# Performance work log

Measured on AMD Instinct MI355X. Metric: run time of the kernel, lower is better.

Reference implementation:

```python
import jax, jax.numpy as jnp
import numpy as np

DIM = 2048
N_HEADS = 16
N_KV_HEADS = 4
HEAD_DIM = DIM // N_HEADS


def setup_inputs() -> dict:
    key = jax.random.key(0)
    k1, k2, k3, k4, k5 = jax.random.split(key, 5)
    B, T = 2, 2048
    scale = 1.0 / np.sqrt(DIM)
    x = jax.random.normal(k1, (B, T, DIM), dtype=jnp.float32)
    # weights stored as [in, out] so forward is x @ W (same math as nn.Linear)
    Wq = jax.random.normal(k2, (DIM, DIM), dtype=jnp.float32) * scale
    Wk = jax.random.normal(k3, (DIM, N_KV_HEADS * HEAD_DIM), dtype=jnp.float32) * scale
    Wv = jax.random.normal(k4, (DIM, N_KV_HEADS * HEAD_DIM), dtype=jnp.float32) * scale
    Wo = jax.random.normal(k5, (DIM, DIM), dtype=jnp.float32) * scale
    return {"x": x, "Wq": Wq, "Wk": Wk, "Wv": Wv, "Wo": Wo}


def reference(x, Wq, Wk, Wv, Wo):
    B, T, C = x.shape
    G = N_HEADS // N_KV_HEADS  # query heads per kv head
    # projections
    q = (x @ Wq).reshape(B, T, N_KV_HEADS, G, HEAD_DIM)   # [B,T,K,G,d]
    k = (x @ Wk).reshape(B, T, N_KV_HEADS, HEAD_DIM)      # [B,T,K,d]
    v = (x @ Wv).reshape(B, T, N_KV_HEADS, HEAD_DIM)      # [B,T,K,d]
    # attention scores: grouped heads share kv head (no repeat_interleave copy)
    att = jnp.einsum('btkgd,bskd->bkgts', q, k) / np.sqrt(HEAD_DIM)  # [B,K,G,T,T]
    att = jax.nn.softmax(att, axis=-1)
    out = jnp.einsum('bkgts,bskd->btkgd', att, v).reshape(B, T, C)
    return out @ Wo
```

## Files before the change

### kernel.cpp

```cpp
#include <hip/hip_runtime.h>
#include <hip/hip_bf16.h>

typedef __hip_bfloat16 bf16;
typedef __attribute__((ext_vector_type(8))) short short8;
typedef __attribute__((ext_vector_type(4))) short short4v;
typedef __attribute__((ext_vector_type(4))) float f32x4;

#define DIMC 2048
#define TSEQ 2048
#define NB 2
#define KVH 4
#define NH 16
#define HD 128
#define KVD 512
#define QSCALE 0.12751744f

__device__ __forceinline__ void mfma16(f32x4& acc, short8 a, short8 b) {
  acc = __builtin_amdgcn_mfma_f32_16x16x32_bf16(a, b, acc, 0, 0, 0);
}

__device__ __forceinline__ void gload_lds16(const bf16* g, bf16* l) {
  __builtin_amdgcn_global_load_lds(
      (const __attribute__((address_space(1))) void*)g,
      (__attribute__((address_space(3))) void*)l, 16, 0, 0);
}

__device__ __forceinline__ int swz(int row, int col) {
  return col ^ ((row & 7) << 3);
}

__global__ __launch_bounds__(256) void f2b(const float* __restrict__ in,
                                           bf16* __restrict__ out, long n4) {
  long i = (long)blockIdx.x * 256 + threadIdx.x;
  if (i >= n4) return;
  const f32x4 v = *(const f32x4*)(in + i * 4);
  union { short4v s; bf16 h[4]; } u;
#pragma unroll
  for (int j = 0; j < 4; ++j) u.h[j] = __float2bfloat16(v[j]);
  *(short4v*)(out + i * 4) = u.s;
}

__global__ __launch_bounds__(256) void transpose_w_f2b(const float* __restrict__ in,
                                                       bf16* __restrict__ out, int C,
                                                       float scale) {
  __shared__ bf16 tile[64][72];
  int rb = blockIdx.y * 64, cb = blockIdx.x * 64;
  int tx = threadIdx.x & 63, ty = threadIdx.x >> 6;
  for (int i = ty; i < 64; i += 4)
    tile[i][tx] = __float2bfloat16(in[(long)(rb + i) * C + cb + tx] * scale);
  __syncthreads();
  for (int i = ty; i < 64; i += 4)
    out[(long)(cb + i) * DIMC + rb + tx] = tile[tx][i];
}

#define GEMM_BODY(A_, Bt_, K_)                                                  \
  const int tid = threadIdx.x;                                                  \
  const int lane = tid & 63, wid = tid >> 6;                                    \
  const long m0 = blockIdx.y * 128, n0 = blockIdx.x * 128;                      \
  const int wm = (wid >> 1) * 64, wn = (wid & 1) * 64;                          \
  f32x4 acc[4][4] = {};                                                         \
  const int srow = lane >> 2, scol = (lane & 3) * 8;                            \
  const bf16* Ag = A_ + (m0 + srow) * (long)K_ + scol;                          \
  const bf16* Bg = Bt_ + (n0 + srow) * (long)K_ + scol;                         \
  for (int k0 = 0; k0 < K_; k0 += 32) {                                         \
    for (int p = 0; p < 2; ++p) {                                               \
      int rr = p * 64 + wid * 16;                                               \
      gload_lds16(Ag + (long)rr * K_ + k0, As + rr * 32);                       \
      gload_lds16(Bg + (long)rr * K_ + k0, Bs + rr * 32);                       \
    }                                                                           \
    __syncthreads();                                                            \
    const int ko = (lane >> 4) * 8;                                             \
    short8 af[4], bq[4];                                                        \
    _Pragma("unroll") for (int i = 0; i < 4; ++i) {                             \
      af[i] = *(const short8*)(As + (wm + i * 16 + (lane & 15)) * 32 + ko);     \
      bq[i] = *(const short8*)(Bs + (wn + i * 16 + (lane & 15)) * 32 + ko);     \
    }                                                                           \
    _Pragma("unroll") for (int i = 0; i < 4; ++i)                               \
      _Pragma("unroll") for (int j = 0; j < 4; ++j)                             \
        mfma16(acc[i][j], af[i], bq[j]);                                        \
    __syncthreads();                                                            \
  }                                                                             \
  const int cr = (lane >> 4) * 4, cc = lane & 15;

__global__ __launch_bounds__(256) void gemm_qkv(const bf16* __restrict__ A,
                                                const bf16* __restrict__ Bt,
                                                bf16* __restrict__ qp,
                                                bf16* __restrict__ kp,
                                                bf16* __restrict__ vT) {
  __shared__ bf16 As[128 * 32];
  __shared__ bf16 Bs[128 * 32];
  GEMM_BODY(A, Bt, 2048)
#pragma unroll
  for (int i = 0; i < 4; ++i)
#pragma unroll
    for (int j = 0; j < 4; ++j)
#pragma unroll
      for (int r = 0; r < 4; ++r) {
        long m = m0 + wm + i * 16 + cr + r;
        long n = n0 + wn + j * 16 + cc;
        float val = acc[i][j][r];
        if (n0 < 2048) {
          qp[m * DIMC + n] = __float2bfloat16(val);
        } else if (n0 < 2560) {
          kp[m * KVD + (n - 2048)] = __float2bfloat16(val);
        } else {
          long nn = n - 2560;
          long z = (m >> 11) * 4 + (nn >> 7);
          vT[z * (HD * (long)TSEQ) + (nn & 127) * (long)TSEQ + (m & 2047)] =
              __float2bfloat16(val);
        }
      }
}

__global__ __launch_bounds__(256) void gemm_out(const bf16* __restrict__ A,
                                                const bf16* __restrict__ Bt,
                                                float* __restrict__ C) {
  __shared__ bf16 As[128 * 32];
  __shared__ bf16 Bs[128 * 32];
  GEMM_BODY(A, Bt, 2048)
#pragma unroll
  for (int i = 0; i < 4; ++i)
#pragma unroll
    for (int j = 0; j < 4; ++j)
#pragma unroll
      for (int r = 0; r < 4; ++r) {
        long m = m0 + wm + i * 16 + cr + r;
        long n = n0 + wn + j * 16 + cc;
        C[m * DIMC + n] = acc[i][j][r];
      }
}

__global__ __launch_bounds__(512, 4) void attn_fwd(const bf16* __restrict__ Qp,
                                                   const bf16* __restrict__ Kp,
                                                   const bf16* __restrict__ Vt,
                                                   bf16* __restrict__ AO) {
  __shared__ bf16 Ks[2][64 * 128];
  __shared__ bf16 Vts[2][128 * 64];
  const int tid = threadIdx.x;
  const int lane = tid & 63, wid = tid >> 6;
  const int h = blockIdx.y, b = blockIdx.z;
  const int kv = h >> 2;
  const int t0 = blockIdx.x * 128;
  const int lr = lane & 15, lg = lane >> 4;

  short8 aq[4];
  {
    const bf16* qrow =
        Qp + ((long)(b * TSEQ + t0 + wid * 16 + lr)) * DIMC + h * HD + lg * 8;
#pragma unroll
    for (int c = 0; c < 4; ++c) aq[c] = *(const short8*)(qrow + c * 32);
  }
  f32x4 o[8] = {};
  float mrun = -1e30f, lrun = 0.f;

  const bf16* Kg = Kp + (long)b * TSEQ * KVD + kv * HD;
  const bf16* Vg = Vt + ((long)(b * KVH + kv)) * HD * TSEQ;

  const int krow = tid >> 3, kc0 = (tid & 7) * 16;
  const int vrow = tid >> 2, va = tid & 3;
  short8 kreg[2], vreg[2];
#pragma unroll
  for (int p = 0; p < 2; ++p) {
    kreg[p] = *(const short8*)(Kg + (long)krow * KVD + kc0 + p * 8);
    vreg[p] = *(const short8*)(Vg + (long)vrow * TSEQ + (va * 16 + 8 * p));
  }

  for (int s0 = 0; s0 < TSEQ; s0 += 64) {
    const int buf = (s0 >> 6) & 1;
    bf16* Kb = Ks[buf];
    bf16* Vb = Vts[buf];
#pragma unroll
    for (int p = 0; p < 2; ++p) {
      *(short8*)(Kb + krow * 128 + swz(krow, kc0 + p * 8)) = kreg[p];
      union { short8 s; short4v q[2]; } u;
      u.s = vreg[p];
      int sl1 = (4 * (va >> 1) + 2 * p + vrow) & 7;
      int sl2 = (4 * (va >> 1) + 2 * p + 1 + vrow) & 7;
      int hf = (va & 1) * 4;
      *(short4v*)(Vb + vrow * 64 + sl1 * 8 + hf) = u.q[0];
      *(short4v*)(Vb + vrow * 64 + sl2 * 8 + hf) = u.q[1];
    }
    __syncthreads();
    if (s0 + 64 < TSEQ) {
#pragma unroll
      for (int p = 0; p < 2; ++p) {
        kreg[p] = *(const short8*)(Kg + (long)(s0 + 64 + krow) * KVD + kc0 + p * 8);
        vreg[p] = *(const short8*)(Vg + (long)vrow * TSEQ + s0 + 64 + (va * 16 + 8 * p));
      }
    }

    f32x4 sacc[4] = {};
    __builtin_amdgcn_s_setprio(1);
#pragma unroll
    for (int sf = 0; sf < 4; ++sf)
#pragma unroll
      for (int c = 0; c < 4; ++c) {
        int row = sf * 16 + lr;
        short8 kf = *(const short8*)(Kb + row * 128 + swz(row, c * 32 + lg * 8));
        mfma16(sacc[sf], kf, aq[c]);
      }
    __builtin_amdgcn_s_setprio(0);

    float tmax = sacc[0][0];
#pragma unroll
    for (int sf = 0; sf < 4; ++sf)
#pragma unroll
      for (int r = 0; r < 4; ++r) tmax = fmaxf(tmax, sacc[sf][r]);
    tmax = fmaxf(tmax, __shfl_xor(tmax, 16));
    tmax = fmaxf(tmax, __shfl_xor(tmax, 32));
    if (__any(tmax > mrun + 8.0f)) {
      float mnew = fmaxf(mrun, tmax);
      float fac = exp2f(mrun - mnew);
      mrun = mnew;
      lrun *= fac;
#pragma unroll
      for (int df = 0; df < 8; ++df) o[df] *= fac;
    }
    float p4[4][4];
    float ps = 0.f;
#pragma unroll
    for (int sf = 0; sf < 4; ++sf)
#pragma unroll
      for (int r = 0; r < 4; ++r) {
        float pv = exp2f(sacc[sf][r] - mrun);
        p4[sf][r] = pv;
        ps += pv;
      }
    ps += __shfl_xor(ps, 16);
    ps += __shfl_xor(ps, 32);
    lrun += ps;

    union { short8 s; bf16 h[8]; } pb[2];
#pragma unroll
    for (int c2 = 0; c2 < 2; ++c2)
#pragma unroll
      for (int r = 0; r < 4; ++r) {
        pb[c2].h[r] = __float2bfloat16(p4[2 * c2][r]);
        pb[c2].h[4 + r] = __float2bfloat16(p4[2 * c2 + 1][r]);
      }

    __builtin_amdgcn_s_setprio(1);
#pragma unroll
    for (int c2 = 0; c2 < 2; ++c2) {
#pragma unroll
      for (int df = 0; df < 8; ++df) {
        int row = df * 16 + lr;
        short8 vf = *(const short8*)(Vb + row * 64 + ((4 * c2 + lg + row) & 7) * 8);
        mfma16(o[df], vf, pb[c2].s);
      }
    }
    __builtin_amdgcn_s_setprio(0);
  }

  float inv = 1.0f / lrun;
  bf16* obase =
      AO + ((long)(b * TSEQ + t0 + wid * 16 + lr)) * DIMC + h * HD + lg * 4;
#pragma unroll
  for (int df = 0; df < 8; ++df) {
    union { short4v s; bf16 h[4]; } ov;
#pragma unroll
    for (int r = 0; r < 4; ++r) ov.h[r] = __float2bfloat16(o[df][r] * inv);
    *(short4v*)(obase + df * 16) = ov.s;
  }
}

extern "C" void kernel_launch(void* const* d_in, const int* in_sizes, int n_in,
                              void* d_out, int out_size, void* d_ws, size_t ws_size,
                              hipStream_t stream) {
  const float* x  = (const float*)d_in[0];
  const float* Wq = (const float*)d_in[1];
  const float* Wk = (const float*)d_in[2];
  const float* Wv = (const float*)d_in[3];
  const float* Wo = (const float*)d_in[4];
  float* out = (float*)d_out;
  bf16* ws = (bf16*)d_ws;

  bf16* xb  = ws;
  bf16* WT3 = xb + 8388608;
  bf16* qp  = WT3 + 6291456;
  bf16* kp  = qp + 8388608;
  bf16* vT  = kp + 2097152;

  f2b<<<8192, 256, 0, stream>>>(x, xb, 2097152);
  transpose_w_f2b<<<dim3(32, 32), 256, 0, stream>>>(Wq, WT3, 2048, QSCALE);
  transpose_w_f2b<<<dim3(8, 32), 256, 0, stream>>>(Wk, WT3 + (long)2048 * 2048, 512, 1.0f);
  transpose_w_f2b<<<dim3(8, 32), 256, 0, stream>>>(Wv, WT3 + (long)2560 * 2048, 512, 1.0f);

  gemm_qkv<<<dim3(24, 32), 256, 0, stream>>>(xb, WT3, qp, kp, vT);

  transpose_w_f2b<<<dim3(32, 32), 256, 0, stream>>>(Wo, WT3, 2048, 1.0f);

  bf16* ao = xb;
  attn_fwd<<<dim3(16, 16, 2), 512, 0, stream>>>(qp, kp, vT, ao);

  gemm_out<<<dim3(16, 32), 256, 0, stream>>>(ao, WT3, out);
}
```

Baseline: 243.3 us.

## Process two query fragments per wave in attention and merge weight transposes

The attention kernel now gives each wave 32 query rows (two 16-row fragments) instead of 16, so every K and V fragment read from LDS feeds two MFMAs. This halves K/V global and LDS traffic per query and halves the grid to 256 blocks, with the launch-bounds occupancy hint lowered from 4 to 2 to make room for the doubled accumulator registers. Separately, the four weight-transpose launches are merged into one kernel, and Wo gets its own workspace buffer so it no longer has to wait until after the QKV GEMM. The risks are higher register pressure, lower occupancy and fewer blocks to spread across the compute units.

```diff
diff --git a/kernel.cpp b/kernel.cpp
--- a/kernel.cpp
+++ b/kernel.cpp
@@ -40,11 +40,31 @@
   *(short4v*)(out + i * 4) = u.s;
 }
 
-__global__ __launch_bounds__(256) void transpose_w_f2b(const float* __restrict__ in,
-                                                       bf16* __restrict__ out, int C,
-                                                       float scale) {
+__global__ __launch_bounds__(256) void transpose_all(const float* __restrict__ Wq,
+                                                     const float* __restrict__ Wk,
+                                                     const float* __restrict__ Wv,
+                                                     const float* __restrict__ Wo,
+                                                     bf16* __restrict__ WT3,
+                                                     bf16* __restrict__ WoT) {
   __shared__ bf16 tile[64][72];
-  int rb = blockIdx.y * 64, cb = blockIdx.x * 64;
+  const int y = blockIdx.y;
+  const float* in;
+  bf16* out;
+  int C, rb, cb;
+  float scale = 1.0f;
+  if (y < 32) {
+    in = Wq; out = WT3; C = 2048;
+    rb = y * 64; cb = blockIdx.x * 64; scale = QSCALE;
+  } else if (y < 40) {
+    in = Wk; out = WT3 + (long)2048 * DIMC; C = 512;
+    rb = blockIdx.x * 64; cb = (y - 32) * 64;
+  } else if (y < 48) {
+    in = Wv; out = WT3 + (long)2560 * DIMC; C = 512;
+    rb = blockIdx.x * 64; cb = (y - 40) * 64;
+  } else {
+    in = Wo; out = WoT; C = 2048;
+    rb = (y - 48) * 64; cb = blockIdx.x * 64;
+  }
   int tx = threadIdx.x & 63, ty = threadIdx.x >> 6;
   for (int i = ty; i < 64; i += 4)
     tile[i][tx] = __float2bfloat16(in[(long)(rb + i) * C + cb + tx] * scale);
@@ -130,7 +150,7 @@
       }
 }
 
-__global__ __launch_bounds__(512, 4) void attn_fwd(const bf16* __restrict__ Qp,
+__global__ __launch_bounds__(512, 2) void attn_fwd(const bf16* __restrict__ Qp,
                                                    const bf16* __restrict__ Kp,
                                                    const bf16* __restrict__ Vt,
                                                    bf16* __restrict__ AO) {
@@ -140,18 +160,19 @@
   const int lane = tid & 63, wid = tid >> 6;
   const int h = blockIdx.y, b = blockIdx.z;
   const int kv = h >> 2;
-  const int t0 = blockIdx.x * 128;
+  const int t0 = blockIdx.x * 256;
   const int lr = lane & 15, lg = lane >> 4;
 
-  short8 aq[4];
-  {
+  short8 aq[2][4];
+#pragma unroll
+  for (int f = 0; f < 2; ++f) {
     const bf16* qrow =
-        Qp + ((long)(b * TSEQ + t0 + wid * 16 + lr)) * DIMC + h * HD + lg * 8;
-#pragma unroll
-    for (int c = 0; c < 4; ++c) aq[c] = *(const short8*)(qrow + c * 32);
-  }
-  f32x4 o[8] = {};
-  float mrun = -1e30f, lrun = 0.f;
+        Qp + ((long)(b * TSEQ + t0 + wid * 32 + f * 16 + lr)) * DIMC + h * HD + lg * 8;
+#pragma unroll
+    for (int c = 0; c < 4; ++c) aq[f][c] = *(const short8*)(qrow + c * 32);
+  }
+  f32x4 o[2][8] = {};
+  float mrun[2] = {-1e30f, -1e30f}, lrun[2] = {0.f, 0.f};
 
   const bf16* Kg = Kp + (long)b * TSEQ * KVD + kv * HD;
   const bf16* Vg = Vt + ((long)(b * KVH + kv)) * HD * TSEQ;
@@ -189,7 +210,7 @@
       }
     }
 
-    f32x4 sacc[4] = {};
+    f32x4 sacc[2][4] = {};
     __builtin_amdgcn_s_setprio(1);
 #pragma unroll
     for (int sf = 0; sf < 4; ++sf)
@@ -197,47 +218,50 @@
       for (int c = 0; c < 4; ++c) {
         int row = sf * 16 + lr;
         short8 kf = *(const short8*)(Kb + row * 128 + swz(row, c * 32 + lg * 8));
-        mfma16(sacc[sf], kf, aq[c]);
+        mfma16(sacc[0][sf], kf, aq[0][c]);
+        mfma16(sacc[1][sf], kf, aq[1][c]);
       }
     __builtin_amdgcn_s_setprio(0);
 
-    float tmax = sacc[0][0];
-#pragma unroll
-    for (int sf = 0; sf < 4; ++sf)
-#pragma unroll
-      for (int r = 0; r < 4; ++r) tmax = fmaxf(tmax, sacc[sf][r]);
-    tmax = fmaxf(tmax, __shfl_xor(tmax, 16));
-    tmax = fmaxf(tmax, __shfl_xor(tmax, 32));
-    if (__any(tmax > mrun + 8.0f)) {
-      float mnew = fmaxf(mrun, tmax);
-      float fac = exp2f(mrun - mnew);
-      mrun = mnew;
-      lrun *= fac;
-#pragma unroll
-      for (int df = 0; df < 8; ++df) o[df] *= fac;
-    }
-    float p4[4][4];
-    float ps = 0.f;
-#pragma unroll
-    for (int sf = 0; sf < 4; ++sf)
-#pragma unroll
-      for (int r = 0; r < 4; ++r) {
-        float pv = exp2f(sacc[sf][r] - mrun);
-        p4[sf][r] = pv;
-        ps += pv;
-      }
-    ps += __shfl_xor(ps, 16);
-    ps += __shfl_xor(ps, 32);
-    lrun += ps;
-
-    union { short8 s; bf16 h[8]; } pb[2];
-#pragma unroll
-    for (int c2 = 0; c2 < 2; ++c2)
-#pragma unroll
-      for (int r = 0; r < 4; ++r) {
-        pb[c2].h[r] = __float2bfloat16(p4[2 * c2][r]);
-        pb[c2].h[4 + r] = __float2bfloat16(p4[2 * c2 + 1][r]);
-      }
+    union { short8 s; bf16 h[8]; } pb[2][2];
+#pragma unroll
+    for (int f = 0; f < 2; ++f) {
+      float tmax = sacc[f][0][0];
+#pragma unroll
+      for (int sf = 0; sf < 4; ++sf)
+#pragma unroll
+        for (int r = 0; r < 4; ++r) tmax = fmaxf(tmax, sacc[f][sf][r]);
+      tmax = fmaxf(tmax, __shfl_xor(tmax, 16));
+      tmax = fmaxf(tmax, __shfl_xor(tmax, 32));
+      if (__any(tmax > mrun[f] + 8.0f)) {
+        float mnew = fmaxf(mrun[f], tmax);
+        float fac = exp2f(mrun[f] - mnew);
+        mrun[f] = mnew;
+        lrun[f] *= fac;
+#pragma unroll
+        for (int df = 0; df < 8; ++df) o[f][df] *= fac;
+      }
+      float p4[4][4];
+      float ps = 0.f;
+#pragma unroll
+      for (int sf = 0; sf < 4; ++sf)
+#pragma unroll
+        for (int r = 0; r < 4; ++r) {
+          float pv = exp2f(sacc[f][sf][r] - mrun[f]);
+          p4[sf][r] = pv;
+          ps += pv;
+        }
+      ps += __shfl_xor(ps, 16);
+      ps += __shfl_xor(ps, 32);
+      lrun[f] += ps;
+#pragma unroll
+      for (int c2 = 0; c2 < 2; ++c2)
+#pragma unroll
+        for (int r = 0; r < 4; ++r) {
+          pb[f][c2].h[r] = __float2bfloat16(p4[2 * c2][r]);
+          pb[f][c2].h[4 + r] = __float2bfloat16(p4[2 * c2 + 1][r]);
+        }
+    }
 
     __builtin_amdgcn_s_setprio(1);
 #pragma unroll
@@ -246,21 +270,25 @@
       for (int df = 0; df < 8; ++df) {
         int row = df * 16 + lr;
         short8 vf = *(const short8*)(Vb + row * 64 + ((4 * c2 + lg + row) & 7) * 8);
-        mfma16(o[df], vf, pb[c2].s);
+        mfma16(o[0][df], vf, pb[0][c2].s);
+        mfma16(o[1][df], vf, pb[1][c2].s);
       }
     }
     __builtin_amdgcn_s_setprio(0);
   }
 
-  float inv = 1.0f / lrun;
-  bf16* obase =
-      AO + ((long)(b * TSEQ + t0 + wid * 16 + lr)) * DIMC + h * HD + lg * 4;
-#pragma unroll
-  for (int df = 0; df < 8; ++df) {
-    union { short4v s; bf16 h[4]; } ov;
-#pragma unroll
-    for (int r = 0; r < 4; ++r) ov.h[r] = __float2bfloat16(o[df][r] * inv);
-    *(short4v*)(obase + df * 16) = ov.s;
+#pragma unroll
+  for (int f = 0; f < 2; ++f) {
+    float inv = 1.0f / lrun[f];
+    bf16* obase =
+        AO + ((long)(b * TSEQ + t0 + wid * 32 + f * 16 + lr)) * DIMC + h * HD + lg * 4;
+#pragma unroll
+    for (int df = 0; df < 8; ++df) {
+      union { short4v s; bf16 h[4]; } ov;
+#pragma unroll
+      for (int r = 0; r < 4; ++r) ov.h[r] = __float2bfloat16(o[f][df][r] * inv);
+      *(short4v*)(obase + df * 16) = ov.s;
+    }
   }
 }
 
@@ -277,21 +305,18 @@
 
   bf16* xb  = ws;
   bf16* WT3 = xb + 8388608;
-  bf16* qp  = WT3 + 6291456;
+  bf16* WoT = WT3 + 6291456;
+  bf16* qp  = WoT + 4194304;
   bf16* kp  = qp + 8388608;
   bf16* vT  = kp + 2097152;
 
   f2b<<<8192, 256, 0, stream>>>(x, xb, 2097152);
-  transpose_w_f2b<<<dim3(32, 32), 256, 0, stream>>>(Wq, WT3, 2048, QSCALE);
-  transpose_w_f2b<<<dim3(8, 32), 256, 0, stream>>>(Wk, WT3 + (long)2048 * 2048, 512, 1.0f);
-  transpose_w_f2b<<<dim3(8, 32), 256, 0, stream>>>(Wv, WT3 + (long)2560 * 2048, 512, 1.0f);
+  transpose_all<<<dim3(32, 80), 256, 0, stream>>>(Wq, Wk, Wv, Wo, WT3, WoT);
 
   gemm_qkv<<<dim3(24, 32), 256, 0, stream>>>(xb, WT3, qp, kp, vT);
 
-  transpose_w_f2b<<<dim3(32, 32), 256, 0, stream>>>(Wo, WT3, 2048, 1.0f);
-
   bf16* ao = xb;
-  attn_fwd<<<dim3(16, 16, 2), 512, 0, stream>>>(qp, kp, vT, ao);
-
-  gemm_out<<<dim3(16, 32), 256, 0, stream>>>(ao, WT3, out);
-}
+  attn_fwd<<<dim3(8, 16, 2), 512, 0, stream>>>(qp, kp, vT, ao);
+
+  gemm_out<<<dim3(16, 32), 256, 0, stream>>>(ao, WoT, out);
+}
```

Result: faster. 232.4 us (-4.5%).
